# Performance work log

Hardware: AMD Instinct MI355X
Metric: run time of the kernel (lower is better)

Reference implementation:

```python
import jax, jax.numpy as jnp
import numpy as np

B, L, D = 4096, 200, 256
NUM_ITEMS, NUM_DT = 200000, 64


def setup_inputs() -> dict:
    key = jax.random.key(0)
    k1, k2, k3, k4, k5, k6 = jax.random.split(key, 6)
    items_pad = jax.random.randint(k1, (B, L), 0, NUM_ITEMS)
    dts_pad = jax.random.randint(k2, (B, L), 0, NUM_DT)
    mask = jnp.ones((B, L), dtype=bool)
    pos_items = jax.random.randint(k3, (B,), 0, NUM_ITEMS)
    neg_items = jax.random.randint(k4, (B,), 0, NUM_ITEMS)
    # embedding tables; row 0 zeroed to emulate padding_idx=0
    item_emb = jax.random.normal(k5, (NUM_ITEMS, D), dtype=jnp.float32).at[0].set(0.0)
    dt_gate = jax.random.normal(k6, (NUM_DT, 1), dtype=jnp.float32).at[0].set(0.0)
    raw_tau = jnp.float32(0.0)
    return {"items_pad": items_pad, "dts_pad": dts_pad, "mask": mask,
            "pos_items": pos_items, "neg_items": neg_items,
            "item_emb": item_emb, "dt_gate": dt_gate, "raw_tau": raw_tau}


def reference(items_pad, dts_pad, mask, pos_items, neg_items, item_emb, dt_gate, raw_tau):
    tau = jax.nn.softplus(raw_tau) + 1e-6
    k = item_emb[items_pad]                       # [B,L,D] history item embeddings
    gate = dt_gate[dts_pad, 0]                    # [B,L]  time-gate scalars

    def cand_aware_uservec(cand_items):
        q = item_emb[cand_items]                  # [B,D]
        sim = jnp.einsum('bld,bd->bl', k, q)      # candidate-aware similarity
        logits = jnp.where(mask, sim * gate / tau, -jnp.inf)
        attn = jax.nn.softmax(logits, axis=1)     # [B,L]
        u = jnp.einsum('bl,bld->bd', attn, k)     # weighted sum (bmm)
        return u, attn, q

    u_pos, attn_pos, q_pos = cand_aware_uservec(pos_items)
    u_neg, _, q_neg = cand_aware_uservec(neg_items)
    pos_score = jnp.sum(u_pos * q_pos, axis=-1)   # [B]
    neg_score = jnp.sum(u_neg * q_neg, axis=-1)   # [B]
    return pos_score, neg_score, attn_pos
```

## Files before the change

### kernel.cpp

```cpp
#include <hip/hip_runtime.h>
#include <hip/hip_bf16.h>
#include <math.h>

#define B_ 4096
#define L_ 200
#define D_ 256

__device__ __forceinline__ float bf2f(unsigned short u) {
    union { unsigned int i; float f; } v; v.i = ((unsigned int)u) << 16; return v.f;
}
__device__ __forceinline__ unsigned short f2bf(float f) {
    __hip_bfloat16 h = __float2bfloat16(f);
    return *reinterpret_cast<unsigned short*>(&h);
}

__global__ void sniff_dtype(const unsigned int* __restrict__ w, int* __restrict__ flag) {
    const int t = threadIdx.x;
    const unsigned int x = w[256 + t];
    const float lo = bf2f((unsigned short)(x & 0xFFFFu));
    const bool garbage = !(lo == lo) || fabsf(lo) > 1e3f;
    const unsigned long long m = __ballot(garbage);
    if (t == 0) flag[0] = (__popcll(m) > 8) ? 1 : 0;
}

template <bool F32>
__device__ __forceinline__ void sic_body(
    const int* __restrict__ items, const int* __restrict__ dts,
    const int* __restrict__ pos_items, const int* __restrict__ neg_items,
    const void* __restrict__ item_emb_v, const void* __restrict__ dt_gate_v,
    const void* __restrict__ raw_tau_v, void* __restrict__ out_v)
{
    const int b    = blockIdx.x;
    const int tid  = threadIdx.x;
    const int lane = tid & 63;
    const int wave = tid >> 6;

    __shared__ int   s_items[L_];
    __shared__ float s_gate[L_];
    __shared__ float s_simp[L_], s_simn[L_];
    __shared__ float s_red[16];

    if (tid < L_) {
        s_items[tid] = items[b * L_ + tid];
        const int di = dts[b * L_ + tid];
        if constexpr (F32) s_gate[tid] = ((const float*)dt_gate_v)[di];
        else               s_gate[tid] = bf2f(((const unsigned short*)dt_gate_v)[di]);
    }

    if constexpr (F32) {
        const float* emb = (const float*)item_emb_v;
        float qp[4], qn[4];
        {
            const float4 a = *(const float4*)(emb + (size_t)pos_items[b] * D_ + lane * 4);
            const float4 c = *(const float4*)(emb + (size_t)neg_items[b] * D_ + lane * 4);
            qp[0]=a.x; qp[1]=a.y; qp[2]=a.z; qp[3]=a.w;
            qn[0]=c.x; qn[1]=c.y; qn[2]=c.z; qn[3]=c.w;
        }
        __syncthreads();
        for (int l = wave; l < L_; l += 4) {
            const float4 kv = *(const float4*)(emb + (size_t)s_items[l] * D_ + lane * 4);
            float sp = 0.f, sn = 0.f;
            sp = fmaf(kv.x, qp[0], sp); sn = fmaf(kv.x, qn[0], sn);
            sp = fmaf(kv.y, qp[1], sp); sn = fmaf(kv.y, qn[1], sn);
            sp = fmaf(kv.z, qp[2], sp); sn = fmaf(kv.z, qn[2], sn);
            sp = fmaf(kv.w, qp[3], sp); sn = fmaf(kv.w, qn[3], sn);
#pragma unroll
            for (int off = 32; off; off >>= 1) {
                sp += __shfl_xor(sp, off, 64);
                sn += __shfl_xor(sn, off, 64);
            }
            if (lane == 0) { s_simp[l] = sp; s_simn[l] = sn; }
        }
    } else {
        const unsigned short* emb = (const unsigned short*)item_emb_v;
        const int half = lane >> 5;
        const int hl   = lane & 31;
        float qp[8], qn[8];
        {
            union { uint4 v; unsigned short s[8]; } a, c;
            a.v = *(const uint4*)(emb + (size_t)pos_items[b] * D_ + (size_t)hl * 8);
            c.v = *(const uint4*)(emb + (size_t)neg_items[b] * D_ + (size_t)hl * 8);
#pragma unroll
            for (int i = 0; i < 8; ++i) { qp[i] = bf2f(a.s[i]); qn[i] = bf2f(c.s[i]); }
        }
        __syncthreads();
        for (int l0 = wave * 2; l0 < L_; l0 += 8) {
            const int l = l0 + half;
            union { uint4 v; unsigned short s[8]; } kv;
            kv.v = *(const uint4*)(emb + (size_t)s_items[l] * D_ + (size_t)hl * 8);
            float sp = 0.f, sn = 0.f;
#pragma unroll
            for (int i = 0; i < 8; ++i) {
                const float kf = bf2f(kv.s[i]);
                sp = fmaf(kf, qp[i], sp);
                sn = fmaf(kf, qn[i], sn);
            }
#pragma unroll
            for (int off = 16; off; off >>= 1) {
                sp += __shfl_xor(sp, off, 64);
                sn += __shfl_xor(sn, off, 64);
            }
            if (hl == 0) { s_simp[l] = sp; s_simn[l] = sn; }
        }
    }
    __syncthreads();

    float rt;
    if constexpr (F32) rt = ((const float*)raw_tau_v)[0];
    else               rt = bf2f(((const unsigned short*)raw_tau_v)[0]);
    const float tau     = log1pf(expf(rt)) + 1e-6f;
    const float inv_tau = 1.0f / tau;

    float sp = 0.f, sn = 0.f, lp = -INFINITY, ln_ = -INFINITY;
    if (tid < L_) {
        sp = s_simp[tid]; sn = s_simn[tid];
        const float g = s_gate[tid] * inv_tau;
        lp  = sp * g;
        ln_ = sn * g;
    }

    float mp = lp, mn = ln_;
#pragma unroll
    for (int off = 32; off; off >>= 1) {
        mp = fmaxf(mp, __shfl_xor(mp, off, 64));
        mn = fmaxf(mn, __shfl_xor(mn, off, 64));
    }
    if (lane == 0) { s_red[wave] = mp; s_red[4 + wave] = mn; }
    __syncthreads();
    mp = fmaxf(fmaxf(s_red[0], s_red[1]), fmaxf(s_red[2], s_red[3]));
    mn = fmaxf(fmaxf(s_red[4], s_red[5]), fmaxf(s_red[6], s_red[7]));
    __syncthreads();

    float ep = 0.f, en = 0.f;
    if (tid < L_) { ep = expf(lp - mp); en = expf(ln_ - mn); }
    float v0 = ep, v1 = en, v2 = ep * sp, v3 = en * sn;
#pragma unroll
    for (int off = 32; off; off >>= 1) {
        v0 += __shfl_xor(v0, off, 64);
        v1 += __shfl_xor(v1, off, 64);
        v2 += __shfl_xor(v2, off, 64);
        v3 += __shfl_xor(v3, off, 64);
    }
    if (lane == 0) {
        s_red[wave] = v0; s_red[4 + wave] = v1;
        s_red[8 + wave] = v2; s_red[12 + wave] = v3;
    }
    __syncthreads();
    const float sum_ep  = s_red[0]  + s_red[1]  + s_red[2]  + s_red[3];
    const float sum_en  = s_red[4]  + s_red[5]  + s_red[6]  + s_red[7];
    const float sum_eps = s_red[8]  + s_red[9]  + s_red[10] + s_red[11];
    const float sum_ens = s_red[12] + s_red[13] + s_red[14] + s_red[15];

    if constexpr (F32) {
        float* out = (float*)out_v;
        if (tid < L_) out[2 * B_ + (size_t)b * L_ + tid] = ep / sum_ep;
        if (tid == 0) { out[b] = sum_eps / sum_ep; out[B_ + b] = sum_ens / sum_en; }
    } else {
        unsigned short* out = (unsigned short*)out_v;
        if (tid < L_) out[2 * B_ + (size_t)b * L_ + tid] = f2bf(ep / sum_ep);
        if (tid == 0) { out[b] = f2bf(sum_eps / sum_ep); out[B_ + b] = f2bf(sum_ens / sum_en); }
    }
}

__global__ __launch_bounds__(256) void sic_bf16(
    const int* items, const int* dts, const int* pos_items, const int* neg_items,
    const void* emb, const void* gate, const void* tau, void* out,
    const int* __restrict__ flag)
{
    if (flag[0] != 0) return;
    sic_body<false>(items, dts, pos_items, neg_items, emb, gate, tau, out);
}

__global__ __launch_bounds__(256) void sic_f32(
    const int* items, const int* dts, const int* pos_items, const int* neg_items,
    const void* emb, const void* gate, const void* tau, void* out,
    const int* __restrict__ flag)
{
    if (flag[0] != 1) return;
    sic_body<true>(items, dts, pos_items, neg_items, emb, gate, tau, out);
}

extern "C" void kernel_launch(void* const* d_in, const int* in_sizes, int n_in,
                              void* d_out, int out_size, void* d_ws, size_t ws_size,
                              hipStream_t stream) {
    const int* items     = (const int*)d_in[0];
    const int* dts       = (const int*)d_in[1];
    const int* pos_items = (const int*)d_in[3];
    const int* neg_items = (const int*)d_in[4];
    const void* item_emb = d_in[5];
    const void* dt_gate  = d_in[6];
    const void* raw_tau  = d_in[7];
    int* flag = (int*)d_ws;

    sniff_dtype<<<1, 64, 0, stream>>>((const unsigned int*)item_emb, flag);
    sic_bf16<<<B_, 256, 0, stream>>>(items, dts, pos_items, neg_items,
                                     item_emb, dt_gate, raw_tau, d_out, flag);
    sic_f32<<<B_, 256, 0, stream>>>(items, dts, pos_items, neg_items,
                                    item_emb, dt_gate, raw_tau, d_out, flag);
}
```

Measured before the change: 385.5 us.

## Drop dtype sniffing, use 32-byte loads with two rows per half-wave

Removes the dtype-detection kernel and the bf16 kernel variant, leaving a single fp32 kernel launch. The similarity loop now has each half-wave handle a row using two float4 loads per lane, and processes two rows per iteration with a fixed 50-row partition per wave. This raises memory-level parallelism and cuts launch overhead and early-exit blocks. It assumes fp32 inputs unconditionally, so bf16 input support is lost.

```diff
diff --git a/kernel.cpp b/kernel.cpp
--- a/kernel.cpp
+++ b/kernel.cpp
@@ -1,39 +1,39 @@
 #include <hip/hip_runtime.h>
-#include <hip/hip_bf16.h>
 #include <math.h>
 
 #define B_ 4096
 #define L_ 200
 #define D_ 256
 
-__device__ __forceinline__ float bf2f(unsigned short u) {
-    union { unsigned int i; float f; } v; v.i = ((unsigned int)u) << 16; return v.f;
-}
-__device__ __forceinline__ unsigned short f2bf(float f) {
-    __hip_bfloat16 h = __float2bfloat16(f);
-    return *reinterpret_cast<unsigned short*>(&h);
+__device__ __forceinline__ void dot8(const float* __restrict__ kp,
+                                     const float qp[8], const float qn[8],
+                                     float& sp, float& sn) {
+    const float4 k0 = *(const float4*)kp;
+    const float4 k1 = *(const float4*)(kp + 4);
+    float a = 0.f, c = 0.f;
+    a = fmaf(k0.x, qp[0], a); c = fmaf(k0.x, qn[0], c);
+    a = fmaf(k0.y, qp[1], a); c = fmaf(k0.y, qn[1], c);
+    a = fmaf(k0.z, qp[2], a); c = fmaf(k0.z, qn[2], c);
+    a = fmaf(k0.w, qp[3], a); c = fmaf(k0.w, qn[3], c);
+    a = fmaf(k1.x, qp[4], a); c = fmaf(k1.x, qn[4], c);
+    a = fmaf(k1.y, qp[5], a); c = fmaf(k1.y, qn[5], c);
+    a = fmaf(k1.z, qp[6], a); c = fmaf(k1.z, qn[6], c);
+    a = fmaf(k1.w, qp[7], a); c = fmaf(k1.w, qn[7], c);
+    sp = a; sn = c;
 }
 
-__global__ void sniff_dtype(const unsigned int* __restrict__ w, int* __restrict__ flag) {
-    const int t = threadIdx.x;
-    const unsigned int x = w[256 + t];
-    const float lo = bf2f((unsigned short)(x & 0xFFFFu));
-    const bool garbage = !(lo == lo) || fabsf(lo) > 1e3f;
-    const unsigned long long m = __ballot(garbage);
-    if (t == 0) flag[0] = (__popcll(m) > 8) ? 1 : 0;
-}
-
-template <bool F32>
-__device__ __forceinline__ void sic_body(
+__global__ __launch_bounds__(256) void sic_f32(
     const int* __restrict__ items, const int* __restrict__ dts,
     const int* __restrict__ pos_items, const int* __restrict__ neg_items,
-    const void* __restrict__ item_emb_v, const void* __restrict__ dt_gate_v,
-    const void* __restrict__ raw_tau_v, void* __restrict__ out_v)
+    const float* __restrict__ emb, const float* __restrict__ dt_gate,
+    const float* __restrict__ raw_tau, float* __restrict__ out)
 {
     const int b    = blockIdx.x;
     const int tid  = threadIdx.x;
     const int lane = tid & 63;
     const int wave = tid >> 6;
+    const int half = lane >> 5;
+    const int hl   = lane & 31;
 
     __shared__ int   s_items[L_];
     __shared__ float s_gate[L_];
@@ -42,72 +42,58 @@
 
     if (tid < L_) {
         s_items[tid] = items[b * L_ + tid];
-        const int di = dts[b * L_ + tid];
-        if constexpr (F32) s_gate[tid] = ((const float*)dt_gate_v)[di];
-        else               s_gate[tid] = bf2f(((const unsigned short*)dt_gate_v)[di]);
+        s_gate[tid]  = dt_gate[dts[b * L_ + tid]];
     }
 
-    if constexpr (F32) {
-        const float* emb = (const float*)item_emb_v;
-        float qp[4], qn[4];
-        {
-            const float4 a = *(const float4*)(emb + (size_t)pos_items[b] * D_ + lane * 4);
-            const float4 c = *(const float4*)(emb + (size_t)neg_items[b] * D_ + lane * 4);
-            qp[0]=a.x; qp[1]=a.y; qp[2]=a.z; qp[3]=a.w;
-            qn[0]=c.x; qn[1]=c.y; qn[2]=c.z; qn[3]=c.w;
-        }
-        __syncthreads();
-        for (int l = wave; l < L_; l += 4) {
-            const float4 kv = *(const float4*)(emb + (size_t)s_items[l] * D_ + lane * 4);
-            float sp = 0.f, sn = 0.f;
-            sp = fmaf(kv.x, qp[0], sp); sn = fmaf(kv.x, qn[0], sn);
-            sp = fmaf(kv.y, qp[1], sp); sn = fmaf(kv.y, qn[1], sn);
-            sp = fmaf(kv.z, qp[2], sp); sn = fmaf(kv.z, qn[2], sn);
-            sp = fmaf(kv.w, qp[3], sp); sn = fmaf(kv.w, qn[3], sn);
-#pragma unroll
-            for (int off = 32; off; off >>= 1) {
-                sp += __shfl_xor(sp, off, 64);
-                sn += __shfl_xor(sn, off, 64);
-            }
-            if (lane == 0) { s_simp[l] = sp; s_simn[l] = sn; }
-        }
-    } else {
-        const unsigned short* emb = (const unsigned short*)item_emb_v;
-        const int half = lane >> 5;
-        const int hl   = lane & 31;
-        float qp[8], qn[8];
-        {
-            union { uint4 v; unsigned short s[8]; } a, c;
-            a.v = *(const uint4*)(emb + (size_t)pos_items[b] * D_ + (size_t)hl * 8);
-            c.v = *(const uint4*)(emb + (size_t)neg_items[b] * D_ + (size_t)hl * 8);
-#pragma unroll
-            for (int i = 0; i < 8; ++i) { qp[i] = bf2f(a.s[i]); qn[i] = bf2f(c.s[i]); }
-        }
-        __syncthreads();
-        for (int l0 = wave * 2; l0 < L_; l0 += 8) {
-            const int l = l0 + half;
-            union { uint4 v; unsigned short s[8]; } kv;
-            kv.v = *(const uint4*)(emb + (size_t)s_items[l] * D_ + (size_t)hl * 8);
-            float sp = 0.f, sn = 0.f;
-#pragma unroll
-            for (int i = 0; i < 8; ++i) {
-                const float kf = bf2f(kv.s[i]);
-                sp = fmaf(kf, qp[i], sp);
-                sn = fmaf(kf, qn[i], sn);
-            }
-#pragma unroll
-            for (int off = 16; off; off >>= 1) {
-                sp += __shfl_xor(sp, off, 64);
-                sn += __shfl_xor(sn, off, 64);
-            }
-            if (hl == 0) { s_simp[l] = sp; s_simn[l] = sn; }
-        }
+    float qp[8], qn[8];
+    {
+        const float* pq = emb + (size_t)pos_items[b] * D_ + (size_t)hl * 8;
+        const float* nq = emb + (size_t)neg_items[b] * D_ + (size_t)hl * 8;
+        const float4 a0 = *(const float4*)pq, a1 = *(const float4*)(pq + 4);
+        const float4 c0 = *(const float4*)nq, c1 = *(const float4*)(nq + 4);
+        qp[0]=a0.x; qp[1]=a0.y; qp[2]=a0.z; qp[3]=a0.w;
+        qp[4]=a1.x; qp[5]=a1.y; qp[6]=a1.z; qp[7]=a1.w;
+        qn[0]=c0.x; qn[1]=c0.y; qn[2]=c0.z; qn[3]=c0.w;
+        qn[4]=c1.x; qn[5]=c1.y; qn[6]=c1.z; qn[7]=c1.w;
     }
     __syncthreads();
 
-    float rt;
-    if constexpr (F32) rt = ((const float*)raw_tau_v)[0];
-    else               rt = bf2f(((const unsigned short*)raw_tau_v)[0]);
+    const int base = wave * 50;
+#pragma unroll 2
+    for (int t = 0; t < 12; ++t) {
+        const int r0 = base + 4 * t + 2 * half;
+        const float* k0p = emb + (size_t)s_items[r0]     * D_ + (size_t)hl * 8;
+        const float* k1p = emb + (size_t)s_items[r0 + 1] * D_ + (size_t)hl * 8;
+        float sp0, sn0, sp1, sn1;
+        dot8(k0p, qp, qn, sp0, sn0);
+        dot8(k1p, qp, qn, sp1, sn1);
+#pragma unroll
+        for (int off = 16; off; off >>= 1) {
+            sp0 += __shfl_xor(sp0, off, 64);
+            sn0 += __shfl_xor(sn0, off, 64);
+            sp1 += __shfl_xor(sp1, off, 64);
+            sn1 += __shfl_xor(sn1, off, 64);
+        }
+        if (hl == 0) {
+            s_simp[r0]     = sp0; s_simn[r0]     = sn0;
+            s_simp[r0 + 1] = sp1; s_simn[r0 + 1] = sn1;
+        }
+    }
+    {
+        const int r = base + 48 + half;
+        const float* kp = emb + (size_t)s_items[r] * D_ + (size_t)hl * 8;
+        float sp, sn;
+        dot8(kp, qp, qn, sp, sn);
+#pragma unroll
+        for (int off = 16; off; off >>= 1) {
+            sp += __shfl_xor(sp, off, 64);
+            sn += __shfl_xor(sn, off, 64);
+        }
+        if (hl == 0) { s_simp[r] = sp; s_simn[r] = sn; }
+    }
+    __syncthreads();
+
+    const float rt      = raw_tau[0];
     const float tau     = log1pf(expf(rt)) + 1e-6f;
     const float inv_tau = 1.0f / tau;
 
@@ -142,8 +128,8 @@
         v3 += __shfl_xor(v3, off, 64);
     }
     if (lane == 0) {
-        s_red[wave] = v0; s_red[4 + wave] = v1;
-        s_red[8 + wave] = v2; s_red[12 + wave] = v3;
+        s_red[wave]      = v0; s_red[4 + wave]  = v1;
+        s_red[8 + wave]  = v2; s_red[12 + wave] = v3;
     }
     __syncthreads();
     const float sum_ep  = s_red[0]  + s_red[1]  + s_red[2]  + s_red[3];
@@ -151,33 +137,11 @@
     const float sum_eps = s_red[8]  + s_red[9]  + s_red[10] + s_red[11];
     const float sum_ens = s_red[12] + s_red[13] + s_red[14] + s_red[15];
 
-    if constexpr (F32) {
-        float* out = (float*)out_v;
-        if (tid < L_) out[2 * B_ + (size_t)b * L_ + tid] = ep / sum_ep;
-        if (tid == 0) { out[b] = sum_eps / sum_ep; out[B_ + b] = sum_ens / sum_en; }
-    } else {
-        unsigned short* out = (unsigned short*)out_v;
-        if (tid < L_) out[2 * B_ + (size_t)b * L_ + tid] = f2bf(ep / sum_ep);
-        if (tid == 0) { out[b] = f2bf(sum_eps / sum_ep); out[B_ + b] = f2bf(sum_ens / sum_en); }
+    if (tid < L_) out[2 * B_ + (size_t)b * L_ + tid] = ep / sum_ep;
+    if (tid == 0) {
+        out[b]      = sum_eps / sum_ep;
+        out[B_ + b] = sum_ens / sum_en;
     }
-}
-
-__global__ __launch_bounds__(256) void sic_bf16(
-    const int* items, const int* dts, const int* pos_items, const int* neg_items,
-    const void* emb, const void* gate, const void* tau, void* out,
-    const int* __restrict__ flag)
-{
-    if (flag[0] != 0) return;
-    sic_body<false>(items, dts, pos_items, neg_items, emb, gate, tau, out);
-}
-
-__global__ __launch_bounds__(256) void sic_f32(
-    const int* items, const int* dts, const int* pos_items, const int* neg_items,
-    const void* emb, const void* gate, const void* tau, void* out,
-    const int* __restrict__ flag)
-{
-    if (flag[0] != 1) return;
-    sic_body<true>(items, dts, pos_items, neg_items, emb, gate, tau, out);
 }
 
 extern "C" void kernel_launch(void* const* d_in, const int* in_sizes, int n_in,
@@ -187,14 +151,11 @@
     const int* dts       = (const int*)d_in[1];
     const int* pos_items = (const int*)d_in[3];
     const int* neg_items = (const int*)d_in[4];
-    const void* item_emb = d_in[5];
-    const void* dt_gate  = d_in[6];
-    const void* raw_tau  = d_in[7];
-    int* flag = (int*)d_ws;
+    const float* item_emb = (const float*)d_in[5];
+    const float* dt_gate  = (const float*)d_in[6];
+    const float* raw_tau  = (const float*)d_in[7];
+    float* out = (float*)d_out;
 
-    sniff_dtype<<<1, 64, 0, stream>>>((const unsigned int*)item_emb, flag);
-    sic_bf16<<<B_, 256, 0, stream>>>(items, dts, pos_items, neg_items,
-                                     item_emb, dt_gate, raw_tau, d_out, flag);
     sic_f32<<<B_, 256, 0, stream>>>(items, dts, pos_items, neg_items,
-                                    item_emb, dt_gate, raw_tau, d_out, flag);
+                                    item_emb, dt_gate, raw_tau, out);
 }
```

After: 361.4 us. 6.3% less time.
